# Performance work log

Hardware: AMD Instinct MI355X
Metric: run time of the kernel (lower is better)

## Reference

```python
import jax, jax.numpy as jnp
import numpy as np

DT = 0.1
BOX = 1.0  # WORLD_SIZE
EPS = 1e-6


def range_angle(ang):
    return jnp.mod(ang + jnp.pi, 2.0 * jnp.pi) - jnp.pi


def ekf_step(x, P, a, Y, n1, n2_sigma, n2_kappa, gains, obs_gains):
    # x: (N,5) [px,py,ang,vel,ang_vel]; P: (N,5,5); a: (N,2); Y: (2,N)
    N = x.shape[0]
    dt = DT
    og = obs_gains

    # --- noise-free dynamics (w=0 in original forward) ---
    vel = gains[0] * a[:, 0]
    ang_vel = gains[1] * a[:, 1]
    ang = range_angle(x[:, 2] + ang_vel * dt)
    px = jnp.clip(x[:, 0] + vel * jnp.cos(ang) * dt, -BOX, BOX)
    py = jnp.clip(x[:, 1] + vel * jnp.sin(ang) * dt, -BOX, BOX)
    x_ = jnp.stack([px, py, ang, vel, ang_vel], axis=1)  # (N,5)

    # --- Jacobian A (N,5,5): eye(3) block + two trig entries ---
    d3 = jnp.arange(3)
    A = jnp.zeros((N, 5, 5), x.dtype)
    A = A.at[:, d3, d3].set(1.0)
    A = A.at[:, 0, 2].set(-vel * jnp.sin(ang) * dt)
    A = A.at[:, 1, 2].set(vel * jnp.cos(ang) * dt)

    # --- predict: L is identity in the original code, so L Q L^T = Q ---
    Q = jnp.diag(jnp.exp(2.0 * n1))
    P_ = jnp.einsum('nij,njk,nlk->nil', A, P, A) + Q  # (N,5,5)

    # --- innovation covariance S = H P_ H^T + M R M^T (R = I, M diag) ---
    # H = [0 | diag(og)] so H P_ H^T = diag(og) P_[3:5,3:5] diag(og)
    HPHt = P_[:, 3:5, 3:5] * og[None, :, None] * og[None, None, :]
    m_diag = x_[:, 3:5] ** 2 * jnp.exp(2.0 * n2_kappa) + jnp.exp(2.0 * n2_sigma)
    S = HPHt + m_diag[:, :, None] * jnp.eye(2, dtype=x.dtype)  # (N,2,2)

    # --- explicit 2x2 inverse ---
    sa, sb = S[:, 0, 0], S[:, 0, 1]
    sc, sd = S[:, 1, 0], S[:, 1, 1]
    det = sa * sd - sb * sc
    Sinv = jnp.stack([jnp.stack([sd, -sb], -1), jnp.stack([-sc, sa], -1)], -2)
    Sinv = Sinv / det[:, None, None]

    # --- Kalman gain K = P_ H^T S^{-1} ---
    PHt = P_[:, :, 3:5] * og[None, None, :]  # (N,5,2)
    K = jnp.einsum('nij,njk->nik', PHt, Sinv)  # (N,5,2)

    # --- update ---
    h = og[None, :] * x_[:, 3:5]  # noise-free observations (N,2)
    err = Y.T - h
    x_new = x_ + jnp.einsum('nij,nj->ni', K, err)

    KH = jnp.zeros((N, 5, 5), x.dtype).at[:, :, 3:5].set(K * og[None, None, :])
    I_KH = jnp.eye(5, dtype=x.dtype) - KH
    P_new = jnp.einsum('nij,njk->nik', I_KH, P_)
    P_new = 0.5 * (P_new + jnp.swapaxes(P_new, -1, -2)) + EPS * jnp.eye(5, dtype=x.dtype)
    return x_new, P_new, K


def setup_inputs() -> dict:
    key = jax.random.key(0)
    ks = jax.random.split(key, 6)
    N = 500_000
    x = jax.random.normal(ks[0], (N, 5), jnp.float32)
    # symmetric positive-definite covariances
    Lr = 0.1 * jax.random.normal(ks[1], (N, 5, 5), jnp.float32)
    P = jnp.einsum('nij,nkj->nik', Lr, Lr) + 0.5 * jnp.eye(5, dtype=jnp.float32)
    a = jax.random.normal(ks[2], (N, 2), jnp.float32)
    Y = 0.5 * jax.random.normal(ks[3], (2, N), jnp.float32)
    n1 = jnp.full((5,), -1.0, jnp.float32)
    n2 = jnp.full((4,), -1.0, jnp.float32)
    return {
        'x': x, 'P': P, 'a': a, 'Y': Y,
        'n1': n1,
        'n2_sigma': n2[:2],
        'n2_kappa': n2[2:],
        'gains': jnp.ones((2,), jnp.float32),
        'obs_gains': jnp.ones((2,), jnp.float32),
    }


def reference(x, P, a, Y, n1, n2_sigma, n2_kappa, gains, obs_gains):
    return ekf_step(x, P, a, Y, n1, n2_sigma, n2_kappa, gains, obs_gains)
```

## Files before the change

kernel.cpp:

```cpp
#include <hip/hip_runtime.h>
#include <math.h>
#include <stdint.h>


#define BLK 64
#define OB_X 0
#define OB_P 320
#define OB_K 1920

struct F3 { float a, b, c; };

struct TR {
    float p00,p01,p02,p10,p11,p12,p20,p21,p22;
    float x0,x1,x2,a0,a1,y0,y1;
};

__device__ __forceinline__ void load_tile(TR& r,
    const float* __restrict__ Pg, const float* __restrict__ xg,
    const float* __restrict__ ag, const float* __restrict__ Yg,
    int N, int i) {
    const float* pb = Pg + (size_t)i * 25;
    F3 r0 = *(const F3*)(pb);
    F3 r1 = *(const F3*)(pb + 5);
    F3 r2 = *(const F3*)(pb + 10);
    F3 xx = *(const F3*)(xg + (size_t)i * 5);
    float2 av = *(const float2*)(ag + (size_t)i * 2);
    r.p00 = r0.a; r.p01 = r0.b; r.p02 = r0.c;
    r.p10 = r1.a; r.p11 = r1.b; r.p12 = r1.c;
    r.p20 = r2.a; r.p21 = r2.b; r.p22 = r2.c;
    r.x0 = xx.a; r.x1 = xx.b; r.x2 = xx.c;
    r.a0 = av.x; r.a1 = av.y;
    r.y0 = Yg[i]; r.y1 = Yg[N + i];
}

struct EkfOut {
    float px, py, ang, xn3, xn4;
    float t00, s01, s02, t11, s12, t22, Pn33, Pn44;
    float K30, K41;
};

__device__ __forceinline__ EkfOut ekf_math(
    float x0, float x1, float x2, float a0, float a1, float y0, float y1,
    float p00, float p01, float p02, float p10, float p11, float p12,
    float p20, float p21, float p22,
    float g0, float g1, float og0, float og1,
    float q0, float q1, float q2, float q3, float q4,
    float e2s0, float e2s1, float e2k0, float e2k1)
{
    const float dt = 0.1f;
    const float fPI  = 3.14159265358979323846f;
    const float f2PI = 6.28318530717958647692f;
    const float EPS_ = 1e-6f;

    float vel = g0 * a0, angvel = g1 * a1;

    float ar = x2 + angvel * dt + fPI;
    float w = fmodf(ar, f2PI);
    if (w < 0.0f) w += f2PI;
    float ang = w - fPI;

    float s, c;
    sincosf(ang, &s, &c);

    EkfOut o;
    o.px = fminf(fmaxf(x0 + vel * c * dt, -1.0f), 1.0f);
    o.py = fminf(fmaxf(x1 + vel * s * dt, -1.0f), 1.0f);
    o.ang = ang;

    float m0 = -vel * s * dt, m1 = vel * c * dt;

    float b00 = p00 + m0 * p20, b01 = p01 + m0 * p21, b02 = p02 + m0 * p22;
    float b10 = p10 + m1 * p20, b11 = p11 + m1 * p21, b12 = p12 + m1 * p22;
    float t00 = b00 + m0 * b02, t01 = b01 + m1 * b02;
    float t10 = b10 + m0 * b12, t11 = b11 + m1 * b12;
    float t20 = p20 + m0 * p22, t21 = p21 + m1 * p22, t22 = p22;
    float t02 = b02, t12 = b12;

    t00 += q0; t11 += q1; t22 += q2;
    o.s01 = 0.5f * (t01 + t10);
    o.s02 = 0.5f * (t02 + t20);
    o.s12 = 0.5f * (t12 + t21);
    o.t00 = t00 + EPS_; o.t11 = t11 + EPS_; o.t22 = t22 + EPS_;

    float S00 = q3 * og0 * og0 + vel * vel * e2k0 + e2s0;
    float S11 = q4 * og1 * og1 + angvel * angvel * e2k1 + e2s1;
    o.K30 = q3 * og0 / S00;
    o.K41 = q4 * og1 / S11;

    o.xn3 = vel    + o.K30 * (y0 - og0 * vel);
    o.xn4 = angvel + o.K41 * (y1 - og1 * angvel);
    o.Pn33 = (1.0f - o.K30 * og0) * q3 + EPS_;
    o.Pn44 = (1.0f - o.K41 * og1) * q4 + EPS_;
    return o;
}

__global__ __launch_bounds__(BLK) void ekf_kernel(
    const float* __restrict__ xg, const float* __restrict__ Pg,
    const float* __restrict__ ag, const float* __restrict__ Yg,
    const float* __restrict__ n1, const float* __restrict__ n2s,
    const float* __restrict__ n2k, const float* __restrict__ gains,
    const float* __restrict__ og, float* __restrict__ out, int N)
{
    __shared__ float obuf[2560];

    const int tid = threadIdx.x;
    const int tiles = (N + BLK - 1) / BLK;
    const int G = gridDim.x, blk = blockIdx.x;
    const int qt = tiles / G, rt = tiles % G;
    const int t0 = blk * qt + min(blk, rt);
    const int myTiles = qt + (blk < rt ? 1 : 0);
    if (myTiles <= 0) return;

    const float g0 = gains[0], g1 = gains[1];
    const float og0 = og[0], og1 = og[1];
    const float q0 = expf(2.f * n1[0]), q1 = expf(2.f * n1[1]),
                q2 = expf(2.f * n1[2]), q3 = expf(2.f * n1[3]),
                q4 = expf(2.f * n1[4]);
    const float e2s0 = expf(2.f * n2s[0]), e2s1 = expf(2.f * n2s[1]);
    const float e2k0 = expf(2.f * n2k[0]), e2k1 = expf(2.f * n2k[1]);

    {
        float* pp = obuf + OB_P + tid * 25;
        pp[3] = 0.f; pp[4] = 0.f; pp[8] = 0.f; pp[9] = 0.f;
        pp[13] = 0.f; pp[14] = 0.f;
        pp[15] = 0.f; pp[16] = 0.f; pp[17] = 0.f; pp[19] = 0.f;
        pp[20] = 0.f; pp[21] = 0.f; pp[22] = 0.f; pp[23] = 0.f;
        float* kk = obuf + OB_K + tid * 10;
        kk[0] = 0.f; kk[1] = 0.f; kk[2] = 0.f; kk[3] = 0.f;
        kk[4] = 0.f; kk[5] = 0.f; kk[7] = 0.f; kk[8] = 0.f;
    }

    TR A, B;
    {
        int i0 = t0 * BLK;
        if (i0 + BLK <= N) load_tile(A, Pg, xg, ag, Yg, N, i0 + tid);
    }

    int k = 0;
    auto process = [&](TR& cur, TR& nxt) {
        const int base = (t0 + k) * BLK;
        const int i = base + tid;
        if (base + BLK <= N) {
            if (k + 1 < myTiles) {
                int nb = base + BLK;
                if (nb + BLK <= N) load_tile(nxt, Pg, xg, ag, Yg, N, nb + tid);
            }

            EkfOut o = ekf_math(cur.x0, cur.x1, cur.x2, cur.a0, cur.a1,
                                cur.y0, cur.y1,
                                cur.p00, cur.p01, cur.p02,
                                cur.p10, cur.p11, cur.p12,
                                cur.p20, cur.p21, cur.p22,
                                g0, g1, og0, og1, q0, q1, q2, q3, q4,
                                e2s0, e2s1, e2k0, e2k1);

            float* xx = obuf + OB_X + tid * 5;
            xx[0] = o.px; xx[1] = o.py; xx[2] = o.ang; xx[3] = o.xn3; xx[4] = o.xn4;
            float* pp = obuf + OB_P + tid * 25;
            pp[0] = o.t00; pp[1] = o.s01; pp[2] = o.s02;
            pp[5] = o.s01; pp[6] = o.t11; pp[7] = o.s12;
            pp[10] = o.s02; pp[11] = o.s12; pp[12] = o.t22;
            pp[18] = o.Pn33; pp[24] = o.Pn44;
            float* kk = obuf + OB_K + tid * 10;
            kk[6] = o.K30; kk[9] = o.K41;

            float4* gx4 = (float4*)(out + (size_t)base * 5);
            float4* gp4 = (float4*)(out + (size_t)5 * N + (size_t)base * 25);
            float4* gk4 = (float4*)(out + (size_t)30 * N + (size_t)base * 10);
            const float4* lx4 = (const float4*)(obuf + OB_X);
            const float4* lp4 = (const float4*)(obuf + OB_P);
            const float4* lk4 = (const float4*)(obuf + OB_K);
            gx4[tid] = lx4[tid];
            if (tid < 16) gx4[64 + tid] = lx4[64 + tid];
            #pragma unroll
            for (int j = 0; j < 6; ++j) gp4[j * 64 + tid] = lp4[j * 64 + tid];
            if (tid < 16) gp4[384 + tid] = lp4[384 + tid];
            #pragma unroll
            for (int j = 0; j < 2; ++j) gk4[j * 64 + tid] = lk4[j * 64 + tid];
            if (tid < 32) gk4[128 + tid] = lk4[128 + tid];
        } else {
            if (i < N) {
                const float* pr = Pg + (size_t)i * 25;
                EkfOut o = ekf_math(xg[i * 5 + 0], xg[i * 5 + 1], xg[i * 5 + 2],
                                    ag[i * 2 + 0], ag[i * 2 + 1],
                                    Yg[i], Yg[N + i],
                                    pr[0], pr[1], pr[2], pr[5], pr[6], pr[7],
                                    pr[10], pr[11], pr[12],
                                    g0, g1, og0, og1, q0, q1, q2, q3, q4,
                                    e2s0, e2s1, e2k0, e2k1);
                float* gx = out + (size_t)i * 5;
                gx[0] = o.px; gx[1] = o.py; gx[2] = o.ang; gx[3] = o.xn3; gx[4] = o.xn4;
                float* gp = out + (size_t)5 * N + (size_t)i * 25;
                gp[0] = o.t00; gp[1] = o.s01; gp[2] = o.s02; gp[3] = 0.f; gp[4] = 0.f;
                gp[5] = o.s01; gp[6] = o.t11; gp[7] = o.s12; gp[8] = 0.f; gp[9] = 0.f;
                gp[10] = o.s02; gp[11] = o.s12; gp[12] = o.t22; gp[13] = 0.f; gp[14] = 0.f;
                gp[15] = 0.f; gp[16] = 0.f; gp[17] = 0.f; gp[18] = o.Pn33; gp[19] = 0.f;
                gp[20] = 0.f; gp[21] = 0.f; gp[22] = 0.f; gp[23] = 0.f; gp[24] = o.Pn44;
                float* gk = out + (size_t)30 * N + (size_t)i * 10;
                gk[0] = 0.f; gk[1] = 0.f; gk[2] = 0.f; gk[3] = 0.f; gk[4] = 0.f;
                gk[5] = 0.f; gk[6] = o.K30; gk[7] = 0.f; gk[8] = 0.f; gk[9] = o.K41;
            }
        }
    };

    while (true) {
        process(A, B);
        if (++k >= myTiles) break;
        process(B, A);
        if (++k >= myTiles) break;
    }
}

extern "C" void kernel_launch(void* const* d_in, const int* in_sizes, int n_in,
                              void* d_out, int out_size, void* d_ws, size_t ws_size,
                              hipStream_t stream) {
    const float* x     = (const float*)d_in[0];
    const float* P     = (const float*)d_in[1];
    const float* a     = (const float*)d_in[2];
    const float* Y     = (const float*)d_in[3];
    const float* n1    = (const float*)d_in[4];
    const float* n2s   = (const float*)d_in[5];
    const float* n2k   = (const float*)d_in[6];
    const float* gains = (const float*)d_in[7];
    const float* og    = (const float*)d_in[8];
    const int N = in_sizes[0] / 5;
    const int tiles = (N + BLK - 1) / BLK;
    int G = 2560;
    if (G > tiles) G = tiles;
    ekf_kernel<<<G, BLK, 0, stream>>>(x, P, a, Y, n1, n2s, n2k, gains, og,
                                      (float*)d_out, N);
}
```

Measured before the change: 146.5 us.

## Coalesce input loads via per-wave LDS staging and use 4-wave blocks

Input P and x tiles are now read with fully coalesced float4 loads across the wave, prefetched one tile ahead in registers, then staged through a per-wave LDS slice and read back per element. Blocks grow to 256 threads, four independent waves each owning a contiguous tile range, and the grid shrinks accordingly. The same LDS slice is reused for output staging, so the zero fill of output entries is rewritten every tile instead of once. The aim is to replace strided 12-byte gathers with coalesced wide loads. The cost is more LDS traffic and more registers spent on the larger prefetch buffer.

New measurement: 172.8 us. 17.9% more time.

```diff
diff --git a/kernel.cpp b/kernel.cpp
--- a/kernel.cpp
+++ b/kernel.cpp
@@ -4,33 +4,39 @@
 
 
 #define BLK 64
-#define OB_X 0
-#define OB_P 320
-#define OB_K 1920
-
-struct F3 { float a, b, c; };
-
-struct TR {
-    float p00,p01,p02,p10,p11,p12,p20,p21,p22;
-    float x0,x1,x2,a0,a1,y0,y1;
+#define SLICE_F 2560
+
+struct Pref {
+    float4 p0, p1, p2, p3, p4, p5;
+    float  pr;
+    float4 x4;
+    float  xr;
+    float2 av;
+    float  y0, y1;
 };
 
-__device__ __forceinline__ void load_tile(TR& r,
+__device__ __forceinline__ void load_pref(Pref& r,
     const float* __restrict__ Pg, const float* __restrict__ xg,
     const float* __restrict__ ag, const float* __restrict__ Yg,
-    int N, int i) {
-    const float* pb = Pg + (size_t)i * 25;
-    F3 r0 = *(const F3*)(pb);
-    F3 r1 = *(const F3*)(pb + 5);
-    F3 r2 = *(const F3*)(pb + 10);
-    F3 xx = *(const F3*)(xg + (size_t)i * 5);
-    float2 av = *(const float2*)(ag + (size_t)i * 2);
-    r.p00 = r0.a; r.p01 = r0.b; r.p02 = r0.c;
-    r.p10 = r1.a; r.p11 = r1.b; r.p12 = r1.c;
-    r.p20 = r2.a; r.p21 = r2.b; r.p22 = r2.c;
-    r.x0 = xx.a; r.x1 = xx.b; r.x2 = xx.c;
-    r.a0 = av.x; r.a1 = av.y;
-    r.y0 = Yg[i]; r.y1 = Yg[N + i];
+    int N, int base, int l) {
+    const float4* p4 = (const float4*)(Pg + (size_t)base * 25);
+    r.p0 = p4[0 * 64 + l]; r.p1 = p4[1 * 64 + l]; r.p2 = p4[2 * 64 + l];
+    r.p3 = p4[3 * 64 + l]; r.p4 = p4[4 * 64 + l]; r.p5 = p4[5 * 64 + l];
+    r.pr = (Pg + (size_t)base * 25)[1536 + l];
+    r.x4 = ((const float4*)(xg + (size_t)base * 5))[l];
+    r.xr = (xg + (size_t)base * 5)[256 + l];
+    r.av = ((const float2*)(ag + (size_t)base * 2))[l];
+    r.y0 = Yg[base + l];
+    r.y1 = Yg[N + base + l];
+}
+
+__device__ __forceinline__ void stage_write(const Pref& r, float* s, int l) {
+    float4* s4 = (float4*)s;
+    s4[0 * 64 + l] = r.p0; s4[1 * 64 + l] = r.p1; s4[2 * 64 + l] = r.p2;
+    s4[3 * 64 + l] = r.p3; s4[4 * 64 + l] = r.p4; s4[5 * 64 + l] = r.p5;
+    s[1536 + l] = r.pr;
+    ((float4*)(s + 1600))[l] = r.x4;
+    s[1856 + l] = r.xr;
 }
 
 struct EkfOut {
@@ -94,21 +100,24 @@
     return o;
 }
 
-__global__ __launch_bounds__(BLK) void ekf_kernel(
+__global__ __launch_bounds__(256) void ekf_kernel(
     const float* __restrict__ xg, const float* __restrict__ Pg,
     const float* __restrict__ ag, const float* __restrict__ Yg,
     const float* __restrict__ n1, const float* __restrict__ n2s,
     const float* __restrict__ n2k, const float* __restrict__ gains,
     const float* __restrict__ og, float* __restrict__ out, int N)
 {
-    __shared__ float obuf[2560];
-
+    __shared__ float4 ldsv[4 * (SLICE_F / 4)];
     const int tid = threadIdx.x;
+    const int wv = tid >> 6, l = tid & 63;
+    float* s = (float*)ldsv + wv * SLICE_F;
+
     const int tiles = (N + BLK - 1) / BLK;
-    const int G = gridDim.x, blk = blockIdx.x;
-    const int qt = tiles / G, rt = tiles % G;
-    const int t0 = blk * qt + min(blk, rt);
-    const int myTiles = qt + (blk < rt ? 1 : 0);
+    const int NW = gridDim.x * 4;
+    const int wp = blockIdx.x * 4 + wv;
+    const int qt = tiles / NW, rt = tiles % NW;
+    const int t0 = wp * qt + min(wp, rt);
+    const int myTiles = qt + (wp < rt ? 1 : 0);
     if (myTiles <= 0) return;
 
     const float g0 = gains[0], g1 = gains[1];
@@ -119,66 +128,61 @@
     const float e2s0 = expf(2.f * n2s[0]), e2s1 = expf(2.f * n2s[1]);
     const float e2k0 = expf(2.f * n2k[0]), e2k1 = expf(2.f * n2k[1]);
 
+    Pref A, B;
     {
-        float* pp = obuf + OB_P + tid * 25;
-        pp[3] = 0.f; pp[4] = 0.f; pp[8] = 0.f; pp[9] = 0.f;
-        pp[13] = 0.f; pp[14] = 0.f;
-        pp[15] = 0.f; pp[16] = 0.f; pp[17] = 0.f; pp[19] = 0.f;
-        pp[20] = 0.f; pp[21] = 0.f; pp[22] = 0.f; pp[23] = 0.f;
-        float* kk = obuf + OB_K + tid * 10;
-        kk[0] = 0.f; kk[1] = 0.f; kk[2] = 0.f; kk[3] = 0.f;
-        kk[4] = 0.f; kk[5] = 0.f; kk[7] = 0.f; kk[8] = 0.f;
+        int b0 = t0 * BLK;
+        if (b0 + BLK <= N) load_pref(A, Pg, xg, ag, Yg, N, b0, l);
     }
 
-    TR A, B;
-    {
-        int i0 = t0 * BLK;
-        if (i0 + BLK <= N) load_tile(A, Pg, xg, ag, Yg, N, i0 + tid);
-    }
-
     int k = 0;
-    auto process = [&](TR& cur, TR& nxt) {
+    auto process = [&](Pref& cur, Pref& nxt) {
         const int base = (t0 + k) * BLK;
-        const int i = base + tid;
         if (base + BLK <= N) {
+            stage_write(cur, s, l);
             if (k + 1 < myTiles) {
                 int nb = base + BLK;
-                if (nb + BLK <= N) load_tile(nxt, Pg, xg, ag, Yg, N, nb + tid);
+                if (nb + BLK <= N) load_pref(nxt, Pg, xg, ag, Yg, N, nb, l);
             }
-
-            EkfOut o = ekf_math(cur.x0, cur.x1, cur.x2, cur.a0, cur.a1,
-                                cur.y0, cur.y1,
-                                cur.p00, cur.p01, cur.p02,
-                                cur.p10, cur.p11, cur.p12,
-                                cur.p20, cur.p21, cur.p22,
+            const float* pr = s + l * 25;
+            float p00 = pr[0], p01 = pr[1], p02 = pr[2];
+            float p10 = pr[5], p11 = pr[6], p12 = pr[7];
+            float p20 = pr[10], p21 = pr[11], p22 = pr[12];
+            const float* xr = s + 1600 + l * 5;
+            float x0 = xr[0], x1 = xr[1], x2 = xr[2];
+
+            EkfOut o = ekf_math(x0, x1, x2, cur.av.x, cur.av.y, cur.y0, cur.y1,
+                                p00, p01, p02, p10, p11, p12, p20, p21, p22,
                                 g0, g1, og0, og1, q0, q1, q2, q3, q4,
                                 e2s0, e2s1, e2k0, e2k1);
 
-            float* xx = obuf + OB_X + tid * 5;
+            float* xx = s + l * 5;
             xx[0] = o.px; xx[1] = o.py; xx[2] = o.ang; xx[3] = o.xn3; xx[4] = o.xn4;
-            float* pp = obuf + OB_P + tid * 25;
-            pp[0] = o.t00; pp[1] = o.s01; pp[2] = o.s02;
-            pp[5] = o.s01; pp[6] = o.t11; pp[7] = o.s12;
-            pp[10] = o.s02; pp[11] = o.s12; pp[12] = o.t22;
-            pp[18] = o.Pn33; pp[24] = o.Pn44;
-            float* kk = obuf + OB_K + tid * 10;
-            kk[6] = o.K30; kk[9] = o.K41;
+            float* pp = s + 320 + l * 25;
+            pp[0]  = o.t00; pp[1]  = o.s01; pp[2]  = o.s02; pp[3]  = 0.f; pp[4]  = 0.f;
+            pp[5]  = o.s01; pp[6]  = o.t11; pp[7]  = o.s12; pp[8]  = 0.f; pp[9]  = 0.f;
+            pp[10] = o.s02; pp[11] = o.s12; pp[12] = o.t22; pp[13] = 0.f; pp[14] = 0.f;
+            pp[15] = 0.f;   pp[16] = 0.f;   pp[17] = 0.f;   pp[18] = o.Pn33; pp[19] = 0.f;
+            pp[20] = 0.f;   pp[21] = 0.f;   pp[22] = 0.f;   pp[23] = 0.f;   pp[24] = o.Pn44;
+            float* kk = s + 1920 + l * 10;
+            kk[0] = 0.f; kk[1] = 0.f; kk[2] = 0.f; kk[3] = 0.f; kk[4] = 0.f;
+            kk[5] = 0.f; kk[6] = o.K30; kk[7] = 0.f; kk[8] = 0.f; kk[9] = o.K41;
 
             float4* gx4 = (float4*)(out + (size_t)base * 5);
             float4* gp4 = (float4*)(out + (size_t)5 * N + (size_t)base * 25);
             float4* gk4 = (float4*)(out + (size_t)30 * N + (size_t)base * 10);
-            const float4* lx4 = (const float4*)(obuf + OB_X);
-            const float4* lp4 = (const float4*)(obuf + OB_P);
-            const float4* lk4 = (const float4*)(obuf + OB_K);
-            gx4[tid] = lx4[tid];
-            if (tid < 16) gx4[64 + tid] = lx4[64 + tid];
+            const float4* lx4 = (const float4*)s;
+            const float4* lp4 = (const float4*)(s + 320);
+            const float4* lk4 = (const float4*)(s + 1920);
+            gx4[l] = lx4[l];
+            if (l < 16) gx4[64 + l] = lx4[64 + l];
             #pragma unroll
-            for (int j = 0; j < 6; ++j) gp4[j * 64 + tid] = lp4[j * 64 + tid];
-            if (tid < 16) gp4[384 + tid] = lp4[384 + tid];
+            for (int j = 0; j < 6; ++j) gp4[j * 64 + l] = lp4[j * 64 + l];
+            if (l < 16) gp4[384 + l] = lp4[384 + l];
             #pragma unroll
-            for (int j = 0; j < 2; ++j) gk4[j * 64 + tid] = lk4[j * 64 + tid];
-            if (tid < 32) gk4[128 + tid] = lk4[128 + tid];
+            for (int j = 0; j < 2; ++j) gk4[j * 64 + l] = lk4[j * 64 + l];
+            if (l < 32) gk4[128 + l] = lk4[128 + l];
         } else {
+            const int i = base + l;
             if (i < N) {
                 const float* pr = Pg + (size_t)i * 25;
                 EkfOut o = ekf_math(xg[i * 5 + 0], xg[i * 5 + 1], xg[i * 5 + 2],
@@ -225,8 +229,8 @@
     const float* og    = (const float*)d_in[8];
     const int N = in_sizes[0] / 5;
     const int tiles = (N + BLK - 1) / BLK;
-    int G = 2560;
-    if (G > tiles) G = tiles;
-    ekf_kernel<<<G, BLK, 0, stream>>>(x, P, a, Y, n1, n2s, n2k, gains, og,
+    int G = 768;
+    if (G * 4 > tiles) G = (tiles + 3) / 4;
+    ekf_kernel<<<G, 256, 0, stream>>>(x, P, a, Y, n1, n2s, n2k, gains, og,
                                       (float*)d_out, N);
 }
```
